# Optimization experiments

Hardware: AMD Instinct MI355X
Metric: run time of the kernel (lower is better)

The kernel has to match this reference:

```python
import jax, jax.numpy as jnp
import numpy as np

ABITS = 4
WBITS = 4
BN_EPS = 1e-5


def _ste(x, q):
    # straight-through estimator: forward q, backward identity
    return x + jax.lax.stop_gradient(q - x)


def act_quant(x):
    # unsigned activation quantization to ABITS (clipped-ReLU style, as in NIPQ quantized act)
    levels = (1 << ABITS) - 1  # 15
    xc = jnp.clip(x, 0.0, 1.0)
    q = jnp.round(xc * levels) / levels
    return _ste(xc, q)


def weight_quant(w):
    # symmetric per-tensor weight quantization to WBITS
    n = (1 << (WBITS - 1)) - 1  # 7
    alpha = jnp.max(jnp.abs(w)) + 1e-12
    wc = jnp.clip(w / alpha, -1.0, 1.0)
    q = jnp.round(wc * n) / n * alpha
    return _ste(w, q)


def conv3x3(x, w):
    # NCHW, OIHW, stride 1, padding 1
    return jax.lax.conv_general_dilated(
        x, w, window_strides=(1, 1), padding=((1, 1), (1, 1)),
        dimension_numbers=('NCHW', 'OIHW', 'NCHW'))


def batchnorm(x, gamma, beta):
    # training-mode BN: batch statistics over (N,H,W)
    mean = jnp.mean(x, axis=(0, 2, 3), keepdims=True)
    var = jnp.var(x, axis=(0, 2, 3), keepdims=True)
    xhat = (x - mean) * jax.lax.rsqrt(var + BN_EPS)
    return xhat * gamma[None, :, None, None] + beta[None, :, None, None]


def setup_inputs() -> dict:
    key = jax.random.key(0)
    k = jax.random.split(key, 3)
    C = 128
    x = jax.random.normal(k[0], (64, C, 56, 56), dtype=jnp.float32)
    w1 = jax.random.normal(k[1], (C, C, 3, 3), dtype=jnp.float32) * 0.05
    w2 = jax.random.normal(k[2], (C, C, 3, 3), dtype=jnp.float32) * 0.05
    return {
        'x': x, 'w1': w1, 'w2': w2,
        'gamma1': jnp.ones((C,), jnp.float32), 'beta1': jnp.zeros((C,), jnp.float32),
        'gamma2': jnp.ones((C,), jnp.float32), 'beta2': jnp.zeros((C,), jnp.float32),
    }


def reference(x, w1, w2, gamma1, beta1, gamma2, beta2):
    identity = x
    out = act_quant(x)
    out = conv3x3(out, weight_quant(w1))
    out = batchnorm(out, gamma1, beta1)
    out = act_quant(out)
    out = conv3x3(out, weight_quant(w2))
    out = batchnorm(out, gamma2, beta2)
    return out + identity
```

## Files before the change

kernel.cpp:

```cpp
#include <hip/hip_runtime.h>

#define CH    128
#define IMG   56
#define PADW  58
#define HWSZ  3136
#define NPIX  200704
#define WELEMS 147456
#define BNEPS 1e-5f
#define PADB  430592
#define YOFF  27557888u
#define Y2OFF_B 51380224u
#define WQ1OFF_B 78938112u

#define BPIX   224
#define NBLK   (NPIX / BPIX)
#define STRIPB 44544
#define STRIPC 2784
#define BBASE  44544
#define REDOFF 77312
#define SMEMSZ 78336

typedef float f32x4 __attribute__((ext_vector_type(4)));
typedef int   i32x4 __attribute__((ext_vector_type(4)));
typedef short short8 __attribute__((ext_vector_type(8)));
typedef _Float16 f16;

__device__ __forceinline__ void async16(const void* g, void* l) {
  __builtin_amdgcn_global_load_lds(
      (const __attribute__((address_space(1))) unsigned int*)g,
      (__attribute__((address_space(3))) unsigned int*)l, 16, 0, 0);
}
__device__ __forceinline__ void bn_inline(int lin, const float* stats, const unsigned* abits,
                                          const float* g, const float* b, float* bnpS) {
  if (lin < 128) {
    const float inv = 1.f / (float)NPIX;
    float gs   = (__uint_as_float(*abits) + 1e-12f) * (1.f / 105.f);
    float mean = stats[lin] * inv;
    float var  = fmaxf(stats[CH + lin] * inv - mean * mean, 0.f);
    float sc   = g[lin] * gs * rsqrtf(gs * gs * var + BNEPS);
    bnpS[lin]      = sc;
    bnpS[CH + lin] = b[lin] - sc * mean;
  }
}
__device__ __forceinline__ void halo_zero(unsigned char* qb, int lin) {
  for (int i = lin; i < 1824; i += 256) {
    size_t off;
    if (i < 464)      off = (size_t)i * 16;
    else if (i < 928) off = (size_t)57 * PADW * 128 + (size_t)(i - 464) * 16;
    else {
      int j = i - 928, loc = j >> 3, sub = j & 7;
      int row = 1 + (loc >> 1), col = (loc & 1) ? 57 : 0;
      off = ((size_t)row * PADW + col) * 128 + (size_t)sub * 16;
    }
    *(uint4*)(qb + off) = (uint4){0u, 0u, 0u, 0u};
  }
}

__global__ void k_wmax(const float* __restrict__ w1, const float* __restrict__ w2,
                       unsigned* __restrict__ alpha_bits) {
  int idx = blockIdx.x * 256 + threadIdx.x;
  float m1 = 0.f, m2 = 0.f;
  for (int i = idx; i < WELEMS; i += gridDim.x * 256) {
    m1 = fmaxf(m1, fabsf(w1[i]));
    m2 = fmaxf(m2, fabsf(w2[i]));
  }
#pragma unroll
  for (int off = 32; off > 0; off >>= 1) {
    m1 = fmaxf(m1, __shfl_xor(m1, off));
    m2 = fmaxf(m2, __shfl_xor(m2, off));
  }
  __shared__ float s1[4], s2[4];
  int wave = threadIdx.x >> 6;
  if ((threadIdx.x & 63) == 0) { s1[wave] = m1; s2[wave] = m2; }
  __syncthreads();
  if (threadIdx.x == 0) {
    m1 = fmaxf(fmaxf(s1[0], s1[1]), fmaxf(s1[2], s1[3]));
    m2 = fmaxf(fmaxf(s2[0], s2[1]), fmaxf(s2[2], s2[3]));
    atomicMax(&alpha_bits[0], __float_as_uint(m1));
    atomicMax(&alpha_bits[1], __float_as_uint(m2));
  }
}

__global__ void k_wquant(const float* __restrict__ w1, const float* __restrict__ w2,
                         const unsigned* __restrict__ alpha_bits,
                         unsigned char* __restrict__ wq1, unsigned char* __restrict__ wq2) {
  int idx = blockIdx.x * 256 + threadIdx.x;
  int t = idx >= WELEMS;
  int j = t ? idx - WELEMS : idx;
  int kk  = j >> 14;
  int rem = j & 16383;
  int co = rem >> 7, ci = rem & 127;
  float alpha = __uint_as_float(alpha_bits[t]) + 1e-12f;
  float v  = (t ? w2 : w1)[co * 1152 + ci * 9 + kk];
  float wc = fminf(fmaxf(v / alpha, -1.f), 1.f);
  int q = (int)rintf(wc * 7.f);
  (t ? wq2 : wq1)[j] = (unsigned char)(q & 0xFF);
}

__global__ void k_actq(const float* __restrict__ x, unsigned char* __restrict__ qx) {
  __shared__ float tile[128][33];
  int n = blockIdx.z, p0 = blockIdx.x * 32;
  int tx = threadIdx.x, ty = threadIdx.y, lin = ty * 32 + tx;
  unsigned char* qb = qx + (size_t)n * PADB;
  if (blockIdx.x == 0) halo_zero(qb, lin);
  const float* xs = x + (size_t)n * CH * HWSZ;
#pragma unroll
  for (int r = 0; r < 16; ++r) {
    int c = ty + r * 8;
    float v = xs[(size_t)c * HWSZ + p0 + tx];
    v = fminf(fmaxf(v, 0.f), 1.f);
    tile[c][tx] = rintf(v * 15.f);
  }
  __syncthreads();
  int p = lin >> 3, q8 = lin & 7;
  int pl = p0 + p;
  int h = pl / IMG, w = pl - h * IMG;
  unsigned u[4];
#pragma unroll
  for (int k = 0; k < 4; ++k) {
    unsigned b0 = (unsigned)(int)tile[q8 * 16 + k * 4 + 0][p];
    unsigned b1 = (unsigned)(int)tile[q8 * 16 + k * 4 + 1][p];
    unsigned b2 = (unsigned)(int)tile[q8 * 16 + k * 4 + 2][p];
    unsigned b3 = (unsigned)(int)tile[q8 * 16 + k * 4 + 3][p];
    u[k] = b0 | (b1 << 8) | (b2 << 16) | (b3 << 24);
  }
  *(uint4*)(qb + ((size_t)(h + 1) * PADW + (w + 1)) * 128 + q8 * 16) =
      (uint4){u[0], u[1], u[2], u[3]};
}

#define CONV_SETUP2                                                              \
  const int tid  = threadIdx.x;                                                  \
  const int lane = tid & 63;                                                     \
  const int quad = lane >> 4, lrow = lane & 15;                                  \
  const int m_base = ((tid >> 6) >> 1) * 112, n_base = ((tid >> 6) & 1) * 64;    \
  int sbase[7];                                                                  \
  _Pragma("unroll")                                                              \
  for (int mi = 0; mi < 7; ++mi) {                                               \
    int row = m_base + mi * 16 + lrow;                                           \
    sbase[mi] = (row / 56) * 58 + (row % 56);                                    \
  }                                                                              \
  int boff[4], bldsoff[4];                                                       \
  _Pragma("unroll")                                                              \
  for (int i = 0; i < 4; ++i) {                                                  \
    int c = i * 256 + tid;                                                       \
    int r = c >> 3;                                                              \
    boff[i] = r * 128 + ((c & 7) ^ (r & 7)) * 16;                                \
    bldsoff[i] = (i * 256 + (tid & ~63)) * 16;                                   \
  }                                                                              \
  i32x4 acc[7][4];                                                               \
  _Pragma("unroll")                                                              \
  for (int mi = 0; mi < 7; ++mi)                                                 \
    _Pragma("unroll")                                                            \
    for (int ni = 0; ni < 4; ++ni) acc[mi][ni] = (i32x4){0, 0, 0, 0};

#define CONV_STAGE_PRO(STRIPSRC, WQ)                                             \
  _Pragma("unroll")                                                              \
  for (int it = 0; it < 11; ++it) {                                              \
    int u = it * 256 + tid;                                                      \
    if (u < STRIPC) {                                                            \
      int s = u >> 3, cc = u & 7;                                                \
      async16((STRIPSRC) + s * 128 + ((cc ^ (s & 7)) << 4),                      \
              smem + (it * 256 + (tid & ~63)) * 16);                             \
    }                                                                            \
  }                                                                              \
  _Pragma("unroll")                                                              \
  for (int i = 0; i < 4; ++i) async16((WQ) + boff[i], smem + BBASE + bldsoff[i]);\
  __syncthreads();

#define CONV_KLOOP2(WQ)                                                          \
  _Pragma("unroll")                                                              \
  for (int kk = 0; kk < 9; ++kk) {                                               \
    if (kk < 8) {                                 \
      const int kn = kk + 1;                                                     \
      char* nb = smem + BBASE + ((kn & 1) << 14);                                \
      _Pragma("unroll")                                                          \
      for (int i = 0; i < 4; ++i)                                                \
        async16((WQ) + kn * 16384 + boff[i], nb + bldsoff[i]);                   \
    }                                                                            \
    const char* Bs = smem + BBASE + ((kk & 1) << 14);                            \
    const int dkk = (kk / 3) * 58 + (kk % 3);                                    \
    int aaddr[7];                                                                \
    _Pragma("unroll")                                                            \
    for (int mi = 0; mi < 7; ++mi) {                                             \
      int s = sbase[mi] + dkk;                                                   \
      aaddr[mi] = (s << 7) + ((quad << 4) ^ ((s & 7) << 4));                     \
    }                                                                            \
    __builtin_amdgcn_s_setprio(1);                                               \
    _Pragma("unroll")                                                            \
    for (int j = 0; j < 2; ++j) {                                                \
      i32x4 af[7], bf[4];                                                        \
      _Pragma("unroll")                                                          \
      for (int mi = 0; mi < 7; ++mi)                                             \
        af[mi] = *(const i32x4*)(smem + (aaddr[mi] ^ (j << 6)));                 \
      _Pragma("unroll")                                                          \
      for (int ni = 0; ni < 4; ++ni) {                                           \
        int brow = n_base + ni * 16 + lrow;                                      \
        bf[ni] = *(const i32x4*)(Bs + brow * 128 +                               \
                                 (((j << 6) | (quad << 4)) ^ ((brow & 7) << 4)));\
      }                                                                          \
      _Pragma("unroll")                                                          \
      for (int mi = 0; mi < 7; ++mi)                                             \
        _Pragma("unroll")                                                        \
        for (int ni = 0; ni < 4; ++ni)                                           \
          acc[mi][ni] = __builtin_amdgcn_mfma_i32_16x16x64_i8(af[mi], bf[ni], acc[mi][ni], 0, 0, 0); \
    }                                                                            \
    __builtin_amdgcn_s_setprio(0);                                               \
    __syncthreads();                                                             \
  }

__global__ __launch_bounds__(256, 2)
void k_conv(const unsigned char* __restrict__ act, const unsigned char* __restrict__ wq,
            short* __restrict__ y, float* __restrict__ stats) {
  __shared__ __align__(16) char smem[SMEMSZ];
  const int n = blockIdx.x / 14, br = blockIdx.x % 14;
  const unsigned char* strip = act + (size_t)n * PADB + (size_t)br * 4 * PADW * 128;
  CONV_SETUP2
  CONV_STAGE_PRO(strip, wq)
  CONV_KLOOP2(wq)
  const int pbase = n * HWSZ + br * BPIX;
  float lsum[4] = {0.f, 0.f, 0.f, 0.f}, lsq[4] = {0.f, 0.f, 0.f, 0.f};
#pragma unroll
  for (int mi = 0; mi < 7; ++mi) {
    int prow = pbase + m_base + mi * 16 + quad * 4;
#pragma unroll
    for (int ni = 0; ni < 4; ++ni) {
      int co = n_base + ni * 16 + lrow;
#pragma unroll
      for (int rg = 0; rg < 4; ++rg) {
        float v = (float)acc[mi][ni][rg];
        y[(size_t)(prow + rg) * CH + co] = (short)fminf(fmaxf(v, -32767.f), 32767.f);
        lsum[ni] += v; lsq[ni] += v * v;
      }
    }
  }
#pragma unroll
  for (int ni = 0; ni < 4; ++ni) {
    lsum[ni] += __shfl_xor(lsum[ni], 16); lsum[ni] += __shfl_xor(lsum[ni], 32);
    lsq[ni]  += __shfl_xor(lsq[ni], 16);  lsq[ni]  += __shfl_xor(lsq[ni], 32);
  }
  __syncthreads();
  float* red = (float*)(smem + REDOFF);
  red[tid] = 0.f;
  __syncthreads();
  if (quad == 0) {
#pragma unroll
    for (int ni = 0; ni < 4; ++ni) {
      int co = n_base + ni * 16 + lrow;
      atomicAdd(&red[co], lsum[ni]);
      atomicAdd(&red[CH + co], lsq[ni]);
    }
  }
  __syncthreads();
  atomicAdd(&stats[tid], red[tid]);
}

__global__ void k_bnq(const short* __restrict__ y, const float* __restrict__ stats,
                      const unsigned* __restrict__ abits, const float* __restrict__ g,
                      const float* __restrict__ b, unsigned char* __restrict__ q) {
  __shared__ float bnpS[256];
  int tid = threadIdx.x;
  bn_inline(tid, stats, abits, g, b, bnpS);
  if (blockIdx.x < 64) halo_zero(q + (size_t)blockIdx.x * PADB, tid);
  __syncthreads();
  size_t i = (size_t)blockIdx.x * 256 + tid;
  short8 v = ((const short8*)y)[i];
  int c0 = (int)((i * 8) & (CH - 1));
  int pix = (int)(i >> 4);
  int n = pix / HWSZ, l = pix - n * HWSZ;
  int h = l / IMG, w = l - h * IMG;
  unsigned lo = 0u, hi = 0u;
#pragma unroll
  for (int j = 0; j < 8; ++j) {
    float u = (float)v[j] * bnpS[c0 + j] + bnpS[CH + c0 + j];
    unsigned qv = (unsigned)(int)rintf(fminf(fmaxf(u, 0.f), 1.f) * 15.f);
    if (j < 4) lo |= qv << (8 * j); else hi |= qv << (8 * (j - 4));
  }
  *(uint2*)(q + (size_t)n * PADB + ((h + 1) * PADW + (w + 1)) * 128 + c0) =
      (uint2){lo, hi};
}

__global__ void k_fin(const short* __restrict__ y2, const float* __restrict__ stats,
                      const unsigned* __restrict__ abits, const float* __restrict__ g,
                      const float* __restrict__ b, const float* __restrict__ x,
                      float* __restrict__ out, int img0) {
  __shared__ float bnpS[256];
  __shared__ float tile[128][33];
  int tx = threadIdx.x, ty = threadIdx.y, lin = ty * 32 + tx;
  bn_inline(lin, stats, abits, g, b, bnpS);
  __syncthreads();
  int n = img0 + blockIdx.z, p0 = blockIdx.x * 32;
  int p = lin >> 3, c0 = (lin & 7) * 16;
  const short* ys = y2 + ((size_t)n * HWSZ + p0 + p) * CH + c0;
  short8 v0 = *(const short8*)ys;
  short8 v1 = *(const short8*)(ys + 8);
#pragma unroll
  for (int j = 0; j < 8; ++j) {
    tile[c0 + j][p]     = (float)v0[j] * bnpS[c0 + j]     + bnpS[CH + c0 + j];
    tile[c0 + 8 + j][p] = (float)v1[j] * bnpS[c0 + 8 + j] + bnpS[CH + c0 + 8 + j];
  }
  __syncthreads();
  const float* xs = x + (size_t)n * CH * HWSZ;
  float*       os = out + (size_t)n * CH * HWSZ;
#pragma unroll
  for (int r = 0; r < 16; ++r) {
    int c = ty + r * 8;
    size_t a = (size_t)c * HWSZ + p0 + tx;
    os[a] = tile[c][tx] + xs[a];
  }
}

__global__ __launch_bounds__(256, 2)
void k_conv_out63(const unsigned char* __restrict__ act, const unsigned char* __restrict__ wq,
                  const float* __restrict__ stats, const unsigned* __restrict__ abits,
                  const float* __restrict__ g, const float* __restrict__ b,
                  const float* __restrict__ x, float* __restrict__ out) {
  __shared__ __align__(16) char smem[SMEMSZ];
  __shared__ float bnpS[256];
  bn_inline(threadIdx.x, stats, abits, g, b, bnpS);
  const int br = blockIdx.x;
  const unsigned char* strip = act + (size_t)br * 4 * PADW * 128;
  CONV_SETUP2
  CONV_STAGE_PRO(strip, wq)
  CONV_KLOOP2(wq)
  __syncthreads();
  f16 (*tile)[228] = (f16(*)[228])smem;
#pragma unroll
  for (int ni = 0; ni < 4; ++ni) {
    int co = n_base + ni * 16 + lrow;
    float sc = bnpS[co], sh = bnpS[CH + co];
#pragma unroll
    for (int mi = 0; mi < 7; ++mi) {
      int pr = m_base + mi * 16 + quad * 4;
#pragma unroll
      for (int rg = 0; rg < 4; ++rg)
        tile[co][pr + rg] = (f16)((float)acc[mi][ni][rg] * sc + sh);
    }
  }
  __syncthreads();
  int c = tid >> 1, seg = tid & 1;
  int pl0 = br * BPIX + seg * 112;
  size_t gb = ((size_t)63 * CH + c) * HWSZ + pl0;
  const float* xp = x + gb;
  float* op = out + gb;
  const f16* tr = &tile[c][seg * 112];
#pragma unroll
  for (int j = 0; j < 112; j += 4) {
    f32x4 xv = *(const f32x4*)(xp + j);
    f32x4 ov;
    ov[0] = (float)tr[j]     + xv[0];
    ov[1] = (float)tr[j + 1] + xv[1];
    ov[2] = (float)tr[j + 2] + xv[2];
    ov[3] = (float)tr[j + 3] + xv[3];
    *(f32x4*)(op + j) = ov;
  }
}

extern "C" void kernel_launch(void* const* d_in, const int* in_sizes, int n_in,
                              void* d_out, int out_size, void* d_ws, size_t ws_size,
                              hipStream_t stream) {
  (void)in_sizes; (void)n_in; (void)out_size;
  const float* x  = (const float*)d_in[0];
  const float* w1 = (const float*)d_in[1];
  const float* w2 = (const float*)d_in[2];
  const float* g1 = (const float*)d_in[3];
  const float* b1 = (const float*)d_in[4];
  const float* g2 = (const float*)d_in[5];
  const float* b2 = (const float*)d_in[6];
  float* out = (float*)d_out;

  char* dob = (char*)d_out;
  unsigned char* q1p = (unsigned char*)dob;
  unsigned char* q2p = (unsigned char*)dob;
  short* y1 = (short*)(dob + YOFF);

  char* ws = (char*)d_ws;
  unsigned* alpha_bits = (unsigned*)ws;
  float* stats1 = (float*)(ws + 256);
  float* stats2 = (float*)(ws + 1280);

  const bool bigws = ws_size >= 51679744u;
  unsigned char *wq1, *wq2;
  short* y2;
  if (bigws) {
    wq1 = (unsigned char*)(ws + 4608);
    wq2 = (unsigned char*)(ws + 152064);
    y2  = (short*)(ws + 299520);
  } else {
    wq1 = (unsigned char*)(dob + WQ1OFF_B);
    wq2 = (unsigned char*)(ws + 4608);
    y2  = (short*)(dob + Y2OFF_B);
  }
  unsigned char* q63p = (unsigned char*)(ws + 152064);

  hipMemsetAsync(ws, 0, 4608, stream);
  k_wmax  <<<64, 256, 0, stream>>>(w1, w2, alpha_bits);
  k_wquant<<<2 * WELEMS / 256, 256, 0, stream>>>(w1, w2, alpha_bits, wq1, wq2);
  k_actq  <<<dim3(98, 1, 64), dim3(32, 8), 0, stream>>>(x, q1p);
  k_conv  <<<NBLK, 256, 0, stream>>>(q1p, wq1, y1, stats1);
  k_bnq   <<<NPIX * CH / 2048, 256, 0, stream>>>(y1, stats1, alpha_bits + 0, g1, b1, q2p);
  k_conv  <<<NBLK, 256, 0, stream>>>(q2p, wq2, y2, stats2);

  if (bigws) {
    k_fin <<<dim3(98, 1, 64), dim3(32, 8), 0, stream>>>(y2, stats2, alpha_bits + 1, g2, b2, x, out, 0);
  } else {
    hipMemcpyAsync(q63p, q2p + (size_t)63 * PADB, PADB, hipMemcpyDeviceToDevice, stream);
    k_fin <<<dim3(98, 1, 32), dim3(32, 8), 0, stream>>>(y2, stats2, alpha_bits + 1, g2, b2, x, out, 0);
    k_fin <<<dim3(98, 1, 16), dim3(32, 8), 0, stream>>>(y2, stats2, alpha_bits + 1, g2, b2, x, out, 32);
    k_fin <<<dim3(98, 1,  8), dim3(32, 8), 0, stream>>>(y2, stats2, alpha_bits + 1, g2, b2, x, out, 48);
    k_fin <<<dim3(98, 1,  4), dim3(32, 8), 0, stream>>>(y2, stats2, alpha_bits + 1, g2, b2, x, out, 56);
    k_fin <<<dim3(98, 1,  2), dim3(32, 8), 0, stream>>>(y2, stats2, alpha_bits + 1, g2, b2, x, out, 60);
    k_fin <<<dim3(98, 1,  1), dim3(32, 8), 0, stream>>>(y2, stats2, alpha_bits + 1, g2, b2, x, out, 62);
    k_conv_out63<<<14, 256, 0, stream>>>(q63p, wq2, stats2, alpha_bits + 1, g2, b2, x, out);
  }
}
```

Before: 326.2 us.

## Split conv2 output across workspace to cut fin launches, swizzle conv blocks, widen bnq

The conv kernel now takes two output base pointers with a split image index, so when the workspace is medium-sized the second conv's output can live partly in the workspace. That replaces the cascade of six halving k_fin launches and the separate image-63 conv with two or three launches. Conv blocks are also remapped in an 8-way interleave so neighbouring block IDs land on different images, and k_bnq handles 16 channels per thread with a 16-byte store. These add index arithmetic and more code paths to keep correct.

```diff
diff --git a/kernel.cpp b/kernel.cpp
--- a/kernel.cpp
+++ b/kernel.cpp
@@ -11,6 +11,7 @@
 #define YOFF  27557888u
 #define Y2OFF_B 51380224u
 #define WQ1OFF_B 78938112u
+#define IMGB  802816u
 
 #define BPIX   224
 #define NBLK   (NPIX / BPIX)
@@ -210,14 +211,18 @@
 
 __global__ __launch_bounds__(256, 2)
 void k_conv(const unsigned char* __restrict__ act, const unsigned char* __restrict__ wq,
-            short* __restrict__ y, float* __restrict__ stats) {
+            short* __restrict__ ylo, short* __restrict__ yhi, int nsplit,
+            float* __restrict__ stats) {
   __shared__ __align__(16) char smem[SMEMSZ];
-  const int n = blockIdx.x / 14, br = blockIdx.x % 14;
+  const int bidx = ((blockIdx.x & 7) * 112) + (blockIdx.x >> 3);
+  const int n = bidx / 14, br = bidx % 14;
   const unsigned char* strip = act + (size_t)n * PADB + (size_t)br * 4 * PADW * 128;
   CONV_SETUP2
   CONV_STAGE_PRO(strip, wq)
   CONV_KLOOP2(wq)
-  const int pbase = n * HWSZ + br * BPIX;
+  short* yb = (n < nsplit ? ylo + (size_t)n * HWSZ * CH
+                          : yhi + (size_t)(n - nsplit) * HWSZ * CH);
+  const int pbase = br * BPIX;
   float lsum[4] = {0.f, 0.f, 0.f, 0.f}, lsq[4] = {0.f, 0.f, 0.f, 0.f};
 #pragma unroll
   for (int mi = 0; mi < 7; ++mi) {
@@ -228,7 +233,7 @@
 #pragma unroll
       for (int rg = 0; rg < 4; ++rg) {
         float v = (float)acc[mi][ni][rg];
-        y[(size_t)(prow + rg) * CH + co] = (short)fminf(fmaxf(v, -32767.f), 32767.f);
+        yb[(size_t)(prow + rg) * CH + co] = (short)fminf(fmaxf(v, -32767.f), 32767.f);
         lsum[ni] += v; lsq[ni] += v * v;
       }
     }
@@ -263,23 +268,28 @@
   if (blockIdx.x < 64) halo_zero(q + (size_t)blockIdx.x * PADB, tid);
   __syncthreads();
   size_t i = (size_t)blockIdx.x * 256 + tid;
-  short8 v = ((const short8*)y)[i];
-  int c0 = (int)((i * 8) & (CH - 1));
-  int pix = (int)(i >> 4);
+  short8 v0 = ((const short8*)y)[i * 2];
+  short8 v1 = ((const short8*)y)[i * 2 + 1];
+  int c0 = (int)((i * 16) & (CH - 1));
+  int pix = (int)(i >> 3);
   int n = pix / HWSZ, l = pix - n * HWSZ;
   int h = l / IMG, w = l - h * IMG;
-  unsigned lo = 0u, hi = 0u;
+  unsigned u[4] = {0u, 0u, 0u, 0u};
 #pragma unroll
   for (int j = 0; j < 8; ++j) {
-    float u = (float)v[j] * bnpS[c0 + j] + bnpS[CH + c0 + j];
-    unsigned qv = (unsigned)(int)rintf(fminf(fmaxf(u, 0.f), 1.f) * 15.f);
-    if (j < 4) lo |= qv << (8 * j); else hi |= qv << (8 * (j - 4));
-  }
-  *(uint2*)(q + (size_t)n * PADB + ((h + 1) * PADW + (w + 1)) * 128 + c0) =
-      (uint2){lo, hi};
-}
-
-__global__ void k_fin(const short* __restrict__ y2, const float* __restrict__ stats,
+    float a0 = (float)v0[j] * bnpS[c0 + j] + bnpS[CH + c0 + j];
+    float a1 = (float)v1[j] * bnpS[c0 + 8 + j] + bnpS[CH + c0 + 8 + j];
+    unsigned q0 = (unsigned)(int)rintf(fminf(fmaxf(a0, 0.f), 1.f) * 15.f);
+    unsigned q1 = (unsigned)(int)rintf(fminf(fmaxf(a1, 0.f), 1.f) * 15.f);
+    u[j >> 2]       |= q0 << (8 * (j & 3));
+    u[2 + (j >> 2)] |= q1 << (8 * (j & 3));
+  }
+  *(uint4*)(q + (size_t)n * PADB + ((h + 1) * PADW + (w + 1)) * 128 + c0) =
+      (uint4){u[0], u[1], u[2], u[3]};
+}
+
+__global__ void k_fin(const short* __restrict__ ylo, const short* __restrict__ yhi, int nsplit,
+                      const float* __restrict__ stats,
                       const unsigned* __restrict__ abits, const float* __restrict__ g,
                       const float* __restrict__ b, const float* __restrict__ x,
                       float* __restrict__ out, int img0) {
@@ -290,7 +300,9 @@
   __syncthreads();
   int n = img0 + blockIdx.z, p0 = blockIdx.x * 32;
   int p = lin >> 3, c0 = (lin & 7) * 16;
-  const short* ys = y2 + ((size_t)n * HWSZ + p0 + p) * CH + c0;
+  const short* ybase = (n < nsplit ? ylo + (size_t)n * HWSZ * CH
+                                   : yhi + (size_t)(n - nsplit) * HWSZ * CH);
+  const short* ys = ybase + (size_t)(p0 + p) * CH + c0;
   short8 v0 = *(const short8*)ys;
   short8 v1 = *(const short8*)(ys + 8);
 #pragma unroll
@@ -378,38 +390,51 @@
   float* stats1 = (float*)(ws + 256);
   float* stats2 = (float*)(ws + 1280);
 
-  const bool bigws = ws_size >= 51679744u;
-  unsigned char *wq1, *wq2;
-  short* y2;
-  if (bigws) {
-    wq1 = (unsigned char*)(ws + 4608);
-    wq2 = (unsigned char*)(ws + 152064);
-    y2  = (short*)(ws + 299520);
-  } else {
-    wq1 = (unsigned char*)(dob + WQ1OFF_B);
-    wq2 = (unsigned char*)(ws + 4608);
-    y2  = (short*)(dob + Y2OFF_B);
-  }
-  unsigned char* q63p = (unsigned char*)(ws + 152064);
-
   hipMemsetAsync(ws, 0, 4608, stream);
   k_wmax  <<<64, 256, 0, stream>>>(w1, w2, alpha_bits);
+
+  if (ws_size >= 51679744u) {
+    unsigned char* wq1 = (unsigned char*)(ws + 4608);
+    unsigned char* wq2 = (unsigned char*)(ws + 152064);
+    short* y2 = (short*)(ws + 299520);
+    k_wquant<<<2 * WELEMS / 256, 256, 0, stream>>>(w1, w2, alpha_bits, wq1, wq2);
+    k_actq  <<<dim3(98, 1, 64), dim3(32, 8), 0, stream>>>(x, q1p);
+    k_conv  <<<NBLK, 256, 0, stream>>>(q1p, wq1, y1, y1, 64, stats1);
+    k_bnq   <<<NPIX * CH / 4096, 256, 0, stream>>>(y1, stats1, alpha_bits + 0, g1, b1, q2p);
+    k_conv  <<<NBLK, 256, 0, stream>>>(q2p, wq2, y2, y2, 64, stats2);
+    k_fin   <<<dim3(98, 1, 64), dim3(32, 8), 0, stream>>>(y2, y2, 64, stats2, alpha_bits + 1, g2, b2, x, out, 0);
+    return;
+  }
+
+  unsigned char* wq1 = (unsigned char*)(dob + WQ1OFF_B);
+  unsigned char* wq2 = (unsigned char*)(ws + 4608);
+  short* y2lo = (short*)(dob + Y2OFF_B);
   k_wquant<<<2 * WELEMS / 256, 256, 0, stream>>>(w1, w2, alpha_bits, wq1, wq2);
   k_actq  <<<dim3(98, 1, 64), dim3(32, 8), 0, stream>>>(x, q1p);
-  k_conv  <<<NBLK, 256, 0, stream>>>(q1p, wq1, y1, stats1);
-  k_bnq   <<<NPIX * CH / 2048, 256, 0, stream>>>(y1, stats1, alpha_bits + 0, g1, b1, q2p);
-  k_conv  <<<NBLK, 256, 0, stream>>>(q2p, wq2, y2, stats2);
-
-  if (bigws) {
-    k_fin <<<dim3(98, 1, 64), dim3(32, 8), 0, stream>>>(y2, stats2, alpha_bits + 1, g2, b2, x, out, 0);
+  k_conv  <<<NBLK, 256, 0, stream>>>(q1p, wq1, y1, y1, 64, stats1);
+  k_bnq   <<<NPIX * CH / 4096, 256, 0, stream>>>(y1, stats1, alpha_bits + 0, g1, b1, q2p);
+
+  if (ws_size >= 152064u + 32u * IMGB) {
+    short* y2hi = (short*)(ws + 152064);
+    k_conv <<<NBLK, 256, 0, stream>>>(q2p, wq2, y2lo, y2hi, 32, stats2);
+    k_fin <<<dim3(98, 1, 32), dim3(32, 8), 0, stream>>>(y2lo, y2hi, 32, stats2, alpha_bits + 1, g2, b2, x, out, 0);
+    k_fin <<<dim3(98, 1, 32), dim3(32, 8), 0, stream>>>(y2lo, y2hi, 32, stats2, alpha_bits + 1, g2, b2, x, out, 32);
+  } else if (ws_size >= 152064u + 16u * IMGB) {
+    short* y2hi = (short*)(ws + 152064);
+    k_conv <<<NBLK, 256, 0, stream>>>(q2p, wq2, y2lo, y2hi, 48, stats2);
+    k_fin <<<dim3(98, 1, 32), dim3(32, 8), 0, stream>>>(y2lo, y2hi, 48, stats2, alpha_bits + 1, g2, b2, x, out, 0);
+    k_fin <<<dim3(98, 1, 16), dim3(32, 8), 0, stream>>>(y2lo, y2hi, 48, stats2, alpha_bits + 1, g2, b2, x, out, 32);
+    k_fin <<<dim3(98, 1, 16), dim3(32, 8), 0, stream>>>(y2lo, y2hi, 48, stats2, alpha_bits + 1, g2, b2, x, out, 48);
   } else {
+    unsigned char* q63p = (unsigned char*)(ws + 152064);
+    k_conv <<<NBLK, 256, 0, stream>>>(q2p, wq2, y2lo, y2lo, 64, stats2);
     hipMemcpyAsync(q63p, q2p + (size_t)63 * PADB, PADB, hipMemcpyDeviceToDevice, stream);
-    k_fin <<<dim3(98, 1, 32), dim3(32, 8), 0, stream>>>(y2, stats2, alpha_bits + 1, g2, b2, x, out, 0);
-    k_fin <<<dim3(98, 1, 16), dim3(32, 8), 0, stream>>>(y2, stats2, alpha_bits + 1, g2, b2, x, out, 32);
-    k_fin <<<dim3(98, 1,  8), dim3(32, 8), 0, stream>>>(y2, stats2, alpha_bits + 1, g2, b2, x, out, 48);
-    k_fin <<<dim3(98, 1,  4), dim3(32, 8), 0, stream>>>(y2, stats2, alpha_bits + 1, g2, b2, x, out, 56);
-    k_fin <<<dim3(98, 1,  2), dim3(32, 8), 0, stream>>>(y2, stats2, alpha_bits + 1, g2, b2, x, out, 60);
-    k_fin <<<dim3(98, 1,  1), dim3(32, 8), 0, stream>>>(y2, stats2, alpha_bits + 1, g2, b2, x, out, 62);
+    k_fin <<<dim3(98, 1, 32), dim3(32, 8), 0, stream>>>(y2lo, y2lo, 64, stats2, alpha_bits + 1, g2, b2, x, out, 0);
+    k_fin <<<dim3(98, 1, 16), dim3(32, 8), 0, stream>>>(y2lo, y2lo, 64, stats2, alpha_bits + 1, g2, b2, x, out, 32);
+    k_fin <<<dim3(98, 1,  8), dim3(32, 8), 0, stream>>>(y2lo, y2lo, 64, stats2, alpha_bits + 1, g2, b2, x, out, 48);
+    k_fin <<<dim3(98, 1,  4), dim3(32, 8), 0, stream>>>(y2lo, y2lo, 64, stats2, alpha_bits + 1, g2, b2, x, out, 56);
+    k_fin <<<dim3(98, 1,  2), dim3(32, 8), 0, stream>>>(y2lo, y2lo, 64, stats2, alpha_bits + 1, g2, b2, x, out, 60);
+    k_fin <<<dim3(98, 1,  1), dim3(32, 8), 0, stream>>>(y2lo, y2lo, 64, stats2, alpha_bits + 1, g2, b2, x, out, 62);
     k_conv_out63<<<14, 256, 0, stream>>>(q63p, wq2, stats2, alpha_bits + 1, g2, b2, x, out);
   }
 }
```

Result: no change. 324.5 us, median of 2 (-0.5%).
